# Optimization experiments

Measured on AMD Instinct MI355X. Metric: run time of the kernel, lower is better.

## Reference

```python
import jax, jax.numpy as jnp
import numpy as np

B, D, K, H, W = 2, 512, 32, 64, 64


def setup_inputs() -> dict:
    key = jax.random.key(0)
    k1, k2, k3 = jax.random.split(key, 3)
    X = jax.random.normal(k1, (B, D, H, W), dtype=jnp.float32)
    std1 = 1.0 / (K * D) ** 0.5
    codewords = jax.random.uniform(k2, (K, D), minval=-std1, maxval=std1, dtype=jnp.float32)
    scale = jax.random.uniform(k3, (D, K), minval=-1.0, maxval=0.0, dtype=jnp.float32)
    return {"X": X, "codewords": codewords, "scale": scale}


def reference(X, codewords, scale):
    # X: [B, D, H, W] -> x: [B, N, D], N = H*W
    Bv, Dv = X.shape[0], X.shape[1]
    x = X.reshape(Bv, Dv, -1).transpose(0, 2, 1)            # [B, N, D]
    # broadcast residual: x[b,n,d] - codewords[k,d], scaled per (d,k)
    residual = (x[:, :, :, None] - codewords.T) * scale     # [B, N, D, K]
    # soft assignment over K codewords
    Q = jax.nn.softmax(-0.5 * jnp.sum(residual * residual, axis=2), axis=2)  # [B, N, K]
    # weighted aggregation over N, normalized by per-codeword mass
    Z_num = jnp.einsum('bnk,bndk->bdk', Q, residual)        # [B, D, K]
    Z_ = Z_num / Q.sum(axis=1)[:, None, :]                  # [B, D, K]
    # L2-normalize along D
    Z = Z_ / jnp.sqrt(jnp.sum(Z_ * Z_, axis=1, keepdims=True))
    return (Z, Q)
```

## Files before the change

### kernel.cpp

```cpp
#include <hip/hip_runtime.h>
#include <math.h>

#define B_DIM 2
#define D_DIM 512
#define K_DIM 32
#define N_DIM 4096

#define WS_T_OFF   128
#define WS_MP_OFF  (128 + B_DIM * D_DIM * K_DIM)

__global__ __launch_bounds__(512, 4)
void k_dist_q(const float* __restrict__ X, const float* __restrict__ CW,
              const float* __restrict__ SC, float* __restrict__ Qout,
              float* __restrict__ W)
{
    __shared__ __align__(16) float xlds[16 * 516];
    __shared__ __align__(16) float red[16 * 16 * 36];

    const int tid = threadIdx.x;
    const int b  = blockIdx.x >> 8;
    const int n0 = (blockIdx.x & 255) << 4;
    const int dp = tid & 63;
    const int kw = tid >> 6;
    const int k0 = kw << 2;

    {
        float* T = W + WS_T_OFF;
        if (tid < 64) T[(blockIdx.x << 6) + tid] = 0.f;
        if (blockIdx.x == 0 && tid >= 64 && tid < 129) W[tid - 64] = 0.f;
    }

    const float* xsrc = X + (size_t)b * D_DIM * N_DIM + n0;
#pragma unroll
    for (int j = 0; j < 4; ++j) {
        const int d  = (tid >> 2) + (j << 7);
        const int n4 = (tid & 3) << 2;
        float4 v = *(const float4*)(xsrc + (size_t)d * N_DIM + n4);
        xlds[(n4 + 0) * 516 + d] = v.x;
        xlds[(n4 + 1) * 516 + d] = v.y;
        xlds[(n4 + 2) * 516 + d] = v.z;
        xlds[(n4 + 3) * 516 + d] = v.w;
    }

    float cv[4][8];
#pragma unroll
    for (int kk = 0; kk < 4; ++kk) {
        const float* cr = CW + (k0 + kk) * D_DIM + (dp << 2);
        float4 c0 = *(const float4*)(cr);
        float4 c1 = *(const float4*)(cr + 256);
        cv[kk][0] = c0.x; cv[kk][1] = c0.y; cv[kk][2] = c0.z; cv[kk][3] = c0.w;
        cv[kk][4] = c1.x; cv[kk][5] = c1.y; cv[kk][6] = c1.z; cv[kk][7] = c1.w;
    }
    float Areg[8][4], Breg[8][4], ckp[4];
#pragma unroll
    for (int kk = 0; kk < 4; ++kk) ckp[kk] = 0.f;
#pragma unroll
    for (int dd = 0; dd < 8; ++dd) {
        const int d = (dd < 4) ? ((dp << 2) + dd) : (256 + (dp << 2) + (dd - 4));
        float4 s4 = *(const float4*)(SC + d * K_DIM + k0);
        float sv[4] = {s4.x, s4.y, s4.z, s4.w};
#pragma unroll
        for (int kk = 0; kk < 4; ++kk) {
            float c = cv[kk][dd];
            float a = sv[kk] * sv[kk];
            float t = a * c;
            Areg[dd][kk] = a;
            Breg[dd][kk] = -2.f * t;
            ckp[kk] = fmaf(t, c, ckp[kk]);
        }
    }
    __syncthreads();

#pragma unroll
    for (int n = 0; n < 16; ++n) {
        float dist[4] = {ckp[0], ckp[1], ckp[2], ckp[3]};
        float4 xa = *(const float4*)(&xlds[n * 516 + (dp << 2)]);
        float4 xb = *(const float4*)(&xlds[n * 516 + (dp << 2) + 256]);
        float xv[8] = {xa.x, xa.y, xa.z, xa.w, xb.x, xb.y, xb.z, xb.w};
#pragma unroll
        for (int dd = 0; dd < 8; ++dd) {
            const float x  = xv[dd];
            const float x2 = x * x;
#pragma unroll
            for (int kk = 0; kk < 4; ++kk) {
                dist[kk] = fmaf(Areg[dd][kk], x2, dist[kk]);
                dist[kk] = fmaf(Breg[dd][kk], x,  dist[kk]);
            }
        }
#pragma unroll
        for (int kk = 0; kk < 4; ++kk) {
            dist[kk] += __shfl_xor(dist[kk], 32);
            dist[kk] += __shfl_xor(dist[kk], 16);
        }
        if (dp < 16)
            *(float4*)(&red[(n * 16 + dp) * 36 + k0]) =
                make_float4(dist[0], dist[1], dist[2], dist[3]);
    }
    __syncthreads();

    const int n = tid >> 5;
    const int k = tid & 31;
    float dsum = 0.f;
#pragma unroll
    for (int i = 0; i < 16; ++i) dsum += red[(n * 16 + i) * 36 + k];
    float m = dsum;
#pragma unroll
    for (int mk = 16; mk >= 1; mk >>= 1)
        m = fminf(m, __shfl_xor(m, mk));
    float e = __expf(-0.5f * (dsum - m));
    float ssum = e;
#pragma unroll
    for (int mk = 16; mk >= 1; mk >>= 1)
        ssum += __shfl_xor(ssum, mk);
    float q = __fdividef(e, ssum);
    Qout[((size_t)b * N_DIM + n0 + n) * K_DIM + k] = q;

    __syncthreads();
    xlds[n * 33 + k] = q;
    __syncthreads();
    if (tid < K_DIM) {
        float t = 0.f;
#pragma unroll
        for (int i = 0; i < 16; ++i) t += xlds[i * 33 + tid];
        W[WS_MP_OFF + blockIdx.x * K_DIM + tid] = t;
    }
}

__global__ __launch_bounds__(256, 2)
void k_tacc(const float* __restrict__ X, const float* __restrict__ Qin,
            float* __restrict__ W)
{
    __shared__ __align__(16) float Xs[64 * 68];
    __shared__ __align__(16) float Qs[32 * 68];
    __shared__ __align__(16) float red4[4 * 64 * 36];

    const int tid = threadIdx.x;
    const int bid = blockIdx.x;
    const int ns = bid & 31;
    const int dt = (bid >> 5) & 7;
    const int b  = bid >> 8;
    const int nsub = tid >> 5;
    const int dp = tid & 7;
    const int kp = (tid >> 3) & 3;
    const int wv = tid >> 6;

    float acc[8][8];
#pragma unroll
    for (int i = 0; i < 8; ++i)
#pragma unroll
        for (int j = 0; j < 8; ++j) acc[i][j] = 0.f;

    const float* xsrc = X + ((size_t)b * D_DIM + dt * 64) * N_DIM + ns * 128;
    const float* qsrc = Qin + ((size_t)b * N_DIM + ns * 128) * K_DIM;

    for (int ch = 0; ch < 2; ++ch) {
        __syncthreads();
#pragma unroll
        for (int i = 0; i < 4; ++i) {
            int flat4 = tid + (i << 8);
            int row = flat4 >> 4;
            int c4  = (flat4 & 15) << 2;
            float4 v = *(const float4*)(xsrc + (size_t)row * N_DIM + (ch << 6) + c4);
            *(float4*)(&Xs[row * 68 + c4]) = v;
        }
#pragma unroll
        for (int i = 0; i < 2; ++i) {
            int flat4 = tid + (i << 8);
            int nn = flat4 >> 3;
            int k4 = (flat4 & 7) << 2;
            float4 v = *(const float4*)(qsrc + ((ch << 6) + nn) * K_DIM + k4);
            Qs[(k4 + 0) * 68 + nn] = v.x;
            Qs[(k4 + 1) * 68 + nn] = v.y;
            Qs[(k4 + 2) * 68 + nn] = v.z;
            Qs[(k4 + 3) * 68 + nn] = v.w;
        }
        __syncthreads();
#pragma unroll
        for (int s = 0; s < 2; ++s) {
            const int nb = (nsub << 3) + (s << 2);
            float4 xr[8], qr[8];
#pragma unroll
            for (int i = 0; i < 8; ++i)
                xr[i] = *(const float4*)(&Xs[(dp + (i << 3)) * 68 + nb]);
#pragma unroll
            for (int j = 0; j < 8; ++j)
                qr[j] = *(const float4*)(&Qs[(kp + (j << 2)) * 68 + nb]);
#pragma unroll
            for (int i = 0; i < 8; ++i)
#pragma unroll
                for (int j = 0; j < 8; ++j) {
                    acc[i][j] = fmaf(xr[i].x, qr[j].x, acc[i][j]);
                    acc[i][j] = fmaf(xr[i].y, qr[j].y, acc[i][j]);
                    acc[i][j] = fmaf(xr[i].z, qr[j].z, acc[i][j]);
                    acc[i][j] = fmaf(xr[i].w, qr[j].w, acc[i][j]);
                }
        }
    }
    __syncthreads();
#pragma unroll
    for (int i = 0; i < 8; ++i)
#pragma unroll
        for (int j = 0; j < 8; ++j)
            acc[i][j] += __shfl_xor(acc[i][j], 32);
    if ((tid & 32) == 0) {
#pragma unroll
        for (int i = 0; i < 8; ++i)
#pragma unroll
            for (int j = 0; j < 8; ++j)
                red4[(wv * 64 + dp + (i << 3)) * 36 + kp + (j << 2)] = acc[i][j];
    }
    __syncthreads();
    float* T = W + WS_T_OFF + (((size_t)b * D_DIM + dt * 64) * K_DIM);
#pragma unroll
    for (int e = 0; e < 8; ++e) {
        int flat = tid + (e << 8);
        int dl = flat >> 5;
        int k  = flat & 31;
        float s = red4[(0 * 64 + dl) * 36 + k] + red4[(1 * 64 + dl) * 36 + k]
                + red4[(2 * 64 + dl) * 36 + k] + red4[(3 * 64 + dl) * 36 + k];
        atomicAdd(&T[dl * K_DIM + k], s);
    }
}

__global__ __launch_bounds__(256)
void k_zfin(const float* __restrict__ CW, const float* __restrict__ SC,
            float* __restrict__ W, float* __restrict__ Z)
{
    __shared__ float mred[8][33];
    __shared__ float Msh[K_DIM];
    __shared__ float part[8][33];

    const int tid = threadIdx.x;
    const int b  = blockIdx.x >> 6;
    const int ds = blockIdx.x & 63;
    const int g  = tid >> 5;
    const int d  = (ds << 3) + g;
    const int k  = tid & 31;

    float* nsq = W;
    int*   cnt = (int*)(W + 64);
    const float* T  = W + WS_T_OFF;
    const float* Mp = W + WS_MP_OFF;

    float pm = 0.f;
#pragma unroll
    for (int i = 0; i < 32; ++i)
        pm += Mp[((b << 8) + (g << 5) + i) * K_DIM + k];
    mred[g][k] = pm;
    __syncthreads();
    if (tid < K_DIM) {
        float t = 0.f;
#pragma unroll
        for (int i = 0; i < 8; ++i) t += mred[i][tid];
        Msh[tid] = t;
    }
    __syncthreads();
    const float m = Msh[k];

    const float t = T[((size_t)(b * D_DIM + d)) * K_DIM + k];
    const float c = CW[k * D_DIM + d];
    const float s = SC[d * K_DIM + k];
    const float z = s * (t / m - c);

    part[g][k] = z * z;
    __syncthreads();
    if (tid < K_DIM) {
        float q = 0.f;
#pragma unroll
        for (int i = 0; i < 8; ++i) q += part[i][tid];
        atomicAdd(&nsq[(b << 5) + tid], q);
    }

    __threadfence();
    __syncthreads();
    if (tid == 0) {
        __hip_atomic_fetch_add(cnt, 1, __ATOMIC_ACQ_REL, __HIP_MEMORY_SCOPE_AGENT);
        while (__hip_atomic_load(cnt, __ATOMIC_ACQUIRE, __HIP_MEMORY_SCOPE_AGENT)
               < (int)gridDim.x)
            __builtin_amdgcn_s_sleep(2);
    }
    __syncthreads();

    const float nv = __hip_atomic_load(&nsq[(b << 5) + k], __ATOMIC_RELAXED,
                                       __HIP_MEMORY_SCOPE_AGENT);
    Z[((size_t)(b * D_DIM + d)) * K_DIM + k] = z * rsqrtf(nv);
}

extern "C" void kernel_launch(void* const* d_in, const int* in_sizes, int n_in,
                              void* d_out, int out_size, void* d_ws, size_t ws_size,
                              hipStream_t stream)
{
    const float* X  = (const float*)d_in[0];
    const float* CW = (const float*)d_in[1];
    const float* SC = (const float*)d_in[2];
    float* Z = (float*)d_out;
    float* Q = (float*)d_out + B_DIM * D_DIM * K_DIM;
    float* W = (float*)d_ws;

    k_dist_q<<<512, 512, 0, stream>>>(X, CW, SC, Q, W);
    k_tacc  <<<512, 256, 0, stream>>>(X, Q, W);
    k_zfin  <<<128, 256, 0, stream>>>(CW, SC, W, Z);
}
```

Before: 107.0 us.

## Replace atomic T accumulation with partial buffers and widen per-thread k tile

```diff
diff --git a/kernel.cpp b/kernel.cpp
--- a/kernel.cpp
+++ b/kernel.cpp
@@ -6,10 +6,10 @@
 #define K_DIM 32
 #define N_DIM 4096
 
-#define WS_T_OFF   128
-#define WS_MP_OFF  (128 + B_DIM * D_DIM * K_DIM)
-
-__global__ __launch_bounds__(512, 4)
+#define WS_MP_OFF  128
+#define WS_TP_OFF  (128 + 512 * K_DIM)
+
+__global__ __launch_bounds__(256, 2)
 void k_dist_q(const float* __restrict__ X, const float* __restrict__ CW,
               const float* __restrict__ SC, float* __restrict__ Qout,
               float* __restrict__ W)
@@ -21,19 +21,15 @@
     const int b  = blockIdx.x >> 8;
     const int n0 = (blockIdx.x & 255) << 4;
     const int dp = tid & 63;
-    const int kw = tid >> 6;
-    const int k0 = kw << 2;
-
-    {
-        float* T = W + WS_T_OFF;
-        if (tid < 64) T[(blockIdx.x << 6) + tid] = 0.f;
-        if (blockIdx.x == 0 && tid >= 64 && tid < 129) W[tid - 64] = 0.f;
-    }
+    const int kp = tid >> 6;
+    const int k0 = kp << 3;
+
+    if (blockIdx.x == 0 && tid < 65) W[tid] = 0.f;
 
     const float* xsrc = X + (size_t)b * D_DIM * N_DIM + n0;
 #pragma unroll
-    for (int j = 0; j < 4; ++j) {
-        const int d  = (tid >> 2) + (j << 7);
+    for (int j = 0; j < 8; ++j) {
+        const int d  = (tid >> 2) + (j << 6);
         const int n4 = (tid & 3) << 2;
         float4 v = *(const float4*)(xsrc + (size_t)d * N_DIM + n4);
         xlds[(n4 + 0) * 516 + d] = v.x;
@@ -42,38 +38,40 @@
         xlds[(n4 + 3) * 516 + d] = v.w;
     }
 
-    float cv[4][8];
-#pragma unroll
-    for (int kk = 0; kk < 4; ++kk) {
+    float cv[8][8];
+#pragma unroll
+    for (int kk = 0; kk < 8; ++kk) {
         const float* cr = CW + (k0 + kk) * D_DIM + (dp << 2);
         float4 c0 = *(const float4*)(cr);
         float4 c1 = *(const float4*)(cr + 256);
         cv[kk][0] = c0.x; cv[kk][1] = c0.y; cv[kk][2] = c0.z; cv[kk][3] = c0.w;
         cv[kk][4] = c1.x; cv[kk][5] = c1.y; cv[kk][6] = c1.z; cv[kk][7] = c1.w;
     }
-    float Areg[8][4], Breg[8][4], ckp[4];
-#pragma unroll
-    for (int kk = 0; kk < 4; ++kk) ckp[kk] = 0.f;
+    float Areg[8][8], Breg[8][8], ckp[8];
+#pragma unroll
+    for (int kk = 0; kk < 8; ++kk) ckp[kk] = 0.f;
 #pragma unroll
     for (int dd = 0; dd < 8; ++dd) {
         const int d = (dd < 4) ? ((dp << 2) + dd) : (256 + (dp << 2) + (dd - 4));
-        float4 s4 = *(const float4*)(SC + d * K_DIM + k0);
-        float sv[4] = {s4.x, s4.y, s4.z, s4.w};
-#pragma unroll
-        for (int kk = 0; kk < 4; ++kk) {
+        float4 s0 = *(const float4*)(SC + d * K_DIM + k0);
+        float4 s1 = *(const float4*)(SC + d * K_DIM + k0 + 4);
+        float sv[8] = {s0.x, s0.y, s0.z, s0.w, s1.x, s1.y, s1.z, s1.w};
+#pragma unroll
+        for (int kk = 0; kk < 8; ++kk) {
             float c = cv[kk][dd];
             float a = sv[kk] * sv[kk];
-            float t = a * c;
             Areg[dd][kk] = a;
-            Breg[dd][kk] = -2.f * t;
-            ckp[kk] = fmaf(t, c, ckp[kk]);
+            Breg[dd][kk] = -2.f * a * c;
+            ckp[kk] = fmaf(a * c, c, ckp[kk]);
         }
     }
     __syncthreads();
 
 #pragma unroll
     for (int n = 0; n < 16; ++n) {
-        float dist[4] = {ckp[0], ckp[1], ckp[2], ckp[3]};
+        float dist[8];
+#pragma unroll
+        for (int kk = 0; kk < 8; ++kk) dist[kk] = ckp[kk];
         float4 xa = *(const float4*)(&xlds[n * 516 + (dp << 2)]);
         float4 xb = *(const float4*)(&xlds[n * 516 + (dp << 2) + 256]);
         float xv[8] = {xa.x, xa.y, xa.z, xa.w, xb.x, xb.y, xb.z, xb.w};
@@ -82,41 +80,44 @@
             const float x  = xv[dd];
             const float x2 = x * x;
 #pragma unroll
-            for (int kk = 0; kk < 4; ++kk) {
+            for (int kk = 0; kk < 8; ++kk) {
                 dist[kk] = fmaf(Areg[dd][kk], x2, dist[kk]);
                 dist[kk] = fmaf(Breg[dd][kk], x,  dist[kk]);
             }
         }
 #pragma unroll
-        for (int kk = 0; kk < 4; ++kk) {
+        for (int kk = 0; kk < 8; ++kk) {
             dist[kk] += __shfl_xor(dist[kk], 32);
             dist[kk] += __shfl_xor(dist[kk], 16);
         }
-        if (dp < 16)
-            *(float4*)(&red[(n * 16 + dp) * 36 + k0]) =
-                make_float4(dist[0], dist[1], dist[2], dist[3]);
-    }
-    __syncthreads();
-
-    const int n = tid >> 5;
-    const int k = tid & 31;
-    float dsum = 0.f;
-#pragma unroll
-    for (int i = 0; i < 16; ++i) dsum += red[(n * 16 + i) * 36 + k];
-    float m = dsum;
-#pragma unroll
-    for (int mk = 16; mk >= 1; mk >>= 1)
-        m = fminf(m, __shfl_xor(m, mk));
-    float e = __expf(-0.5f * (dsum - m));
-    float ssum = e;
-#pragma unroll
-    for (int mk = 16; mk >= 1; mk >>= 1)
-        ssum += __shfl_xor(ssum, mk);
-    float q = __fdividef(e, ssum);
-    Qout[((size_t)b * N_DIM + n0 + n) * K_DIM + k] = q;
-
-    __syncthreads();
-    xlds[n * 33 + k] = q;
+        if (dp < 16) {
+            float* r = &red[(n * 16 + dp) * 36 + k0];
+            *(float4*)(r)     = make_float4(dist[0], dist[1], dist[2], dist[3]);
+            *(float4*)(r + 4) = make_float4(dist[4], dist[5], dist[6], dist[7]);
+        }
+    }
+    __syncthreads();
+
+#pragma unroll
+    for (int h = 0; h < 2; ++h) {
+        const int n = (tid >> 5) + (h << 3);
+        const int k = tid & 31;
+        float dsum = 0.f;
+#pragma unroll
+        for (int i = 0; i < 16; ++i) dsum += red[(n * 16 + i) * 36 + k];
+        float m = dsum;
+#pragma unroll
+        for (int mk = 16; mk >= 1; mk >>= 1)
+            m = fminf(m, __shfl_xor(m, mk));
+        float e = __expf(-0.5f * (dsum - m));
+        float ssum = e;
+#pragma unroll
+        for (int mk = 16; mk >= 1; mk >>= 1)
+            ssum += __shfl_xor(ssum, mk);
+        float q = __fdividef(e, ssum);
+        Qout[((size_t)b * N_DIM + n0 + n) * K_DIM + k] = q;
+        xlds[n * 33 + k] = q;
+    }
     __syncthreads();
     if (tid < K_DIM) {
         float t = 0.f;
@@ -127,8 +128,8 @@
 }
 
 __global__ __launch_bounds__(256, 2)
-void k_tacc(const float* __restrict__ X, const float* __restrict__ Qin,
-            float* __restrict__ W)
+void k_tpart(const float* __restrict__ X, const float* __restrict__ Qin,
+             float* __restrict__ W)
 {
     __shared__ __align__(16) float Xs[64 * 68];
     __shared__ __align__(16) float Qs[32 * 68];
@@ -210,7 +211,7 @@
                 red4[(wv * 64 + dp + (i << 3)) * 36 + kp + (j << 2)] = acc[i][j];
     }
     __syncthreads();
-    float* T = W + WS_T_OFF + (((size_t)b * D_DIM + dt * 64) * K_DIM);
+    float* dst = W + WS_TP_OFF + (((size_t)ns * 2 + b) * D_DIM + dt * 64) * K_DIM;
 #pragma unroll
     for (int e = 0; e < 8; ++e) {
         int flat = tid + (e << 8);
@@ -218,7 +219,7 @@
         int k  = flat & 31;
         float s = red4[(0 * 64 + dl) * 36 + k] + red4[(1 * 64 + dl) * 36 + k]
                 + red4[(2 * 64 + dl) * 36 + k] + red4[(3 * 64 + dl) * 36 + k];
-        atomicAdd(&T[dl * K_DIM + k], s);
+        dst[dl * K_DIM + k] = s;
     }
 }
 
@@ -239,8 +240,8 @@
 
     float* nsq = W;
     int*   cnt = (int*)(W + 64);
-    const float* T  = W + WS_T_OFF;
     const float* Mp = W + WS_MP_OFF;
+    const float* TP = W + WS_TP_OFF;
 
     float pm = 0.f;
 #pragma unroll
@@ -257,10 +258,14 @@
     __syncthreads();
     const float m = Msh[k];
 
-    const float t = T[((size_t)(b * D_DIM + d)) * K_DIM + k];
+    float sum = 0.f;
+#pragma unroll
+    for (int ns = 0; ns < 32; ++ns)
+        sum += TP[(((size_t)ns * 2 + b) * D_DIM + d) * K_DIM + k];
+
     const float c = CW[k * D_DIM + d];
     const float s = SC[d * K_DIM + k];
-    const float z = s * (t / m - c);
+    const float z = s * (sum / m - c);
 
     part[g][k] = z * z;
     __syncthreads();
@@ -297,7 +302,7 @@
     float* Q = (float*)d_out + B_DIM * D_DIM * K_DIM;
     float* W = (float*)d_ws;
 
-    k_dist_q<<<512, 512, 0, stream>>>(X, CW, SC, Q, W);
-    k_tacc  <<<512, 256, 0, stream>>>(X, Q, W);
+    k_dist_q<<<512, 256, 0, stream>>>(X, CW, SC, Q, W);
+    k_tpart <<<512, 256, 0, stream>>>(X, Q, W);
     k_zfin  <<<128, 256, 0, stream>>>(CW, SC, W, Z);
 }
```

After: 107.0 us. Within noise of the previous version (-0.0%).
